# Performance work log

Hardware: AMD Instinct MI355X
Metric: run time of the kernel (lower is better)

## Reference

```python
import jax, jax.numpy as jnp
import numpy as np

# Model hyperparams (match init_kwargs)
D_MODEL = 1024
D_STATE = 128
D_CONV = 4
EXPAND = 2
HEADDIM = 64
NGROUPS = 1
D_INNER = EXPAND * D_MODEL          # 2048
D_SSM = D_INNER                     # d_ssm=None -> d_inner; d_mlp = 0
NHEADS = D_SSM // HEADDIM           # 32
CONV_DIM = D_SSM + 2 * NGROUPS * D_STATE            # 2304
D_IN_PROJ = 2 * D_INNER + 2 * NGROUPS * D_STATE + NHEADS  # 4384
GROUP_SIZE = D_SSM // NGROUPS
EPS = 1e-5
HEAD_TO_GROUP = np.arange(NHEADS) // (NHEADS // NGROUPS)


def silu(x):
    return x * jax.nn.sigmoid(x)


def setup_inputs() -> dict:
    key = jax.random.key(0)
    ks = jax.random.split(key, 10)
    B, L = 16, 512
    u = jax.random.normal(ks[0], (B, L, D_MODEL), jnp.float32)
    # in_proj (bias=False): weight [d_in_proj, d_model]
    W_in = jax.random.normal(ks[1], (D_IN_PROJ, D_MODEL), jnp.float32) / np.sqrt(D_MODEL)
    # depthwise causal conv1d: weight [conv_dim, 1, d_conv], bias [conv_dim]
    conv_w = jax.random.normal(ks[2], (CONV_DIM, 1, D_CONV), jnp.float32) / np.sqrt(D_CONV)
    conv_b = jax.random.normal(ks[3], (CONV_DIM,), jnp.float32) * 0.01
    # recurrent feedback weights (zero-init in torch; small random here to exercise the path)
    W_rxbc = jax.random.normal(ks[4], (CONV_DIM, D_SSM), jnp.float32) * (0.01 / np.sqrt(D_SSM))
    W_rdt = jax.random.normal(ks[5], (NHEADS, D_SSM), jnp.float32) * (0.01 / np.sqrt(D_SSM))
    # dt_bias = inverse-softplus of dt ~ U_log[1e-3, 1e-1]
    dt = jnp.exp(jax.random.uniform(ks[6], (NHEADS,)) * (np.log(0.1) - np.log(0.001)) + np.log(0.001))
    dt_bias = dt + jnp.log(-jnp.expm1(-dt))
    A_log = jnp.log(jax.random.uniform(ks[7], (NHEADS,), minval=1.0, maxval=16.0))
    D_param = jnp.ones((NHEADS,), jnp.float32)
    norm_w = jnp.ones((D_SSM,), jnp.float32)
    W_out = jax.random.normal(ks[8], (D_MODEL, D_INNER), jnp.float32) / np.sqrt(D_INNER)
    return dict(u=u, W_in=W_in, conv_w=conv_w, conv_b=conv_b, W_rxbc=W_rxbc,
                W_rdt=W_rdt, dt_bias=dt_bias, A_log=A_log, D_param=D_param,
                norm_w=norm_w, W_out=W_out)


def _forward(u, W_in, conv_w, conv_b, W_rxbc, W_rdt, dt_bias, A_log, D_param, norm_w, W_out):
    B, L, _ = u.shape
    zxbcdt = jnp.einsum('bld,ed->ble', u, W_in)  # [B,L,d_in_proj]; d_mlp=0 so no z0/x0
    z, xBC_u, dt_raw = jnp.split(zxbcdt, [D_SSM, D_SSM + CONV_DIM], axis=-1)
    # causal depthwise conv over time (torch Conv1d pad=d_conv-1, truncated to L)
    xp = jnp.pad(xBC_u, ((0, 0), (D_CONV - 1, 0), (0, 0)))
    xBC_conv = conv_b + sum(xp[:, k:k + L, :] * conv_w[:, 0, k] for k in range(D_CONV))
    A = -jnp.exp(A_log.astype(jnp.float32))  # [H]

    def step(carry, inp):
        state, y_prev = carry            # state: [B,H,P,N] f32, y_prev: [B,d_ssm]
        xBC_t, dt_t, z_t = inp
        xBC = silu(xBC_t + y_prev @ W_rxbc.T)        # recurrent xBC feedback
        dtr = silu(dt_t + y_prev @ W_rdt.T)          # recurrent dt feedback
        x_t = xBC[:, :D_SSM]
        Bv = xBC[:, D_SSM:D_SSM + NGROUPS * D_STATE]
        Cv = xBC[:, D_SSM + NGROUPS * D_STATE:]
        dt = jax.nn.softplus(dtr + dt_bias).astype(jnp.float32)  # [B,H]; dt_limit=(0,inf) -> no clamp
        dA = jnp.exp(dt * A)                                     # [B,H]
        x_h = x_t.reshape(B, NHEADS, HEADDIM).astype(jnp.float32)
        B_hn = Bv.reshape(B, NGROUPS, D_STATE).astype(jnp.float32)[:, HEAD_TO_GROUP, :]
        C_hn = Cv.reshape(B, NGROUPS, D_STATE).astype(jnp.float32)[:, HEAD_TO_GROUP, :]
        state = state * dA[:, :, None, None] + dt[:, :, None, None] * x_h[:, :, :, None] * B_hn[:, :, None, :]
        y = (state * C_hn[:, :, None, :]).sum(-1) + D_param[None, :, None] * x_h  # [B,H,P]
        y = y.reshape(B, D_SSM)
        # gated RMSNorm (norm_before_gate=False): rmsnorm(y*silu(z)) * weight, groupwise
        g = y * silu(z_t)
        gg = g.reshape(B, NGROUPS, GROUP_SIZE)
        ms = jnp.mean(gg * gg, axis=-1, keepdims=True)
        yn = (gg * jax.lax.rsqrt(ms + EPS)).reshape(B, D_SSM) * norm_w
        out_t = yn @ W_out.T
        return (state, yn), out_t

    state0 = jnp.zeros((B, NHEADS, HEADDIM, D_STATE), jnp.float32)
    y0 = jnp.zeros((B, D_SSM), u.dtype)
    xs = (jnp.swapaxes(xBC_conv, 0, 1), jnp.swapaxes(dt_raw, 0, 1), jnp.swapaxes(z, 0, 1))
    _, out = jax.lax.scan(step, (state0, y0), xs)  # out: [L,B,d_model]
    return jnp.swapaxes(out, 0, 1)


def reference(u, W_in, conv_w, conv_b, W_rxbc, W_rdt, dt_bias, A_log, D_param, norm_w, W_out):
    return _forward(u, W_in, conv_w, conv_b, W_rxbc, W_rdt, dt_bias, A_log, D_param, norm_w, W_out)
```

## Files before the change

### kernel.cpp

```cpp
#include <hip/hip_runtime.h>

typedef __attribute__((ext_vector_type(8))) short short8;
typedef __attribute__((ext_vector_type(4))) float floatx4;

#define BQ 16
#define LQ 512
#define DM 1024
#define DPROJ 4384
#define RAWC 2336
#define KD 2048
#define NWG 128
#define NTHR 512
#define AWG 73

#define RAWT_SLOT 37376
#define MSUM_SLOT 512

__device__ __forceinline__ float siluf(float x) { return x / (1.f + __expf(-x)); }
__device__ __forceinline__ float softplusf(float x) { return (x > 20.f) ? x : log1pf(__expf(x)); }
__device__ __forceinline__ unsigned short f2bf(float f) {
    union { float f; unsigned u; } v; v.f = f;
    unsigned r = v.u + 0x7FFFu + ((v.u >> 16) & 1u);
    return (unsigned short)(r >> 16);
}
__device__ __forceinline__ unsigned long long ld64(const unsigned long long* p) {
    return __hip_atomic_load(p, __ATOMIC_RELAXED, __HIP_MEMORY_SCOPE_AGENT);
}
__device__ __forceinline__ void st64(unsigned long long* p, unsigned long long v) {
    __hip_atomic_store(p, v, __ATOMIC_RELAXED, __HIP_MEMORY_SCOPE_AGENT);
}
__device__ __forceinline__ unsigned long long packf(float f, unsigned e) {
    union { float f; unsigned u; } v; v.f = f;
    return ((unsigned long long)e << 32) | v.u;
}
__device__ __forceinline__ float lof(unsigned long long w) {
    union { unsigned u; float f; } v; v.u = (unsigned)w; return v.f;
}
__device__ __forceinline__ unsigned hie(unsigned long long w) { return (unsigned)(w >> 32); }

__global__ void cvt_bf16_kernel(const float* __restrict__ s, unsigned short* __restrict__ d, int n) {
    int i = blockIdx.x * 256 + threadIdx.x;
    if (i < n) d[i] = f2bf(s[i]);
}

__global__ void pack_weights_kernel(const float* __restrict__ rxbc, const float* __restrict__ rdt,
                                    const float* __restrict__ wout, unsigned short* __restrict__ wall) {
    long i = (long)blockIdx.x * 256 + threadIdx.x;
    if (i >= 3360L * KD) return;
    int c = (int)(i >> 11), k = (int)(i & 2047);
    const float* src = (c < 2304) ? rxbc + (long)c * KD + k
                     : (c < 2336) ? rdt + (long)(c - 2304) * KD + k
                     :              wout + (long)(c - 2336) * KD + k;
    wall[i] = f2bf(*src);
}

__global__ void setup_zero_kernel(unsigned* __restrict__ z, long nz, unsigned* __restrict__ gh0) {
    long i = (long)blockIdx.x * 256 + threadIdx.x;
    const long stride = (long)gridDim.x * 256;
    for (long k = i; k < nz; k += stride) z[k] = 0u;
    if (i < 16384) gh0[i] = 0u;
}

__global__ __launch_bounds__(256) void gemm_inproj_kernel(const short* __restrict__ A,
                                                          const short* __restrict__ Bw,
                                                          float* __restrict__ C) {
    const int lane = threadIdx.x & 63, wave = threadIdx.x >> 6;
    const int row = lane & 15, q = lane >> 4;
    const long m0 = (long)blockIdx.x * 128 + wave * 16;
    const long n0 = (long)blockIdx.y * 32;
    const short* ap0 = A + (m0 + row) * DM + q * 8;
    const short* ap1 = ap0 + 64 * DM;
    const short* bp0 = Bw + (n0 + row) * DM + q * 8;
    const short* bp1 = bp0 + 16 * DM;
    floatx4 acc00 = {0.f,0.f,0.f,0.f}, acc01 = {0.f,0.f,0.f,0.f};
    floatx4 acc10 = {0.f,0.f,0.f,0.f}, acc11 = {0.f,0.f,0.f,0.f};
    for (int k = 0; k < DM; k += 32) {
        short8 a0 = *(const short8*)(ap0 + k);
        short8 a1 = *(const short8*)(ap1 + k);
        short8 b0 = *(const short8*)(bp0 + k);
        short8 b1 = *(const short8*)(bp1 + k);
        acc00 = __builtin_amdgcn_mfma_f32_16x16x32_bf16(a0, b0, acc00, 0, 0, 0);
        acc01 = __builtin_amdgcn_mfma_f32_16x16x32_bf16(a0, b1, acc01, 0, 0, 0);
        acc10 = __builtin_amdgcn_mfma_f32_16x16x32_bf16(a1, b0, acc10, 0, 0, 0);
        acc11 = __builtin_amdgcn_mfma_f32_16x16x32_bf16(a1, b1, acc11, 0, 0, 0);
    }
    float* cp0 = C + (m0 + q * 4) * DPROJ + n0 + row;
    float* cp1 = cp0 + 64 * DPROJ;
    #pragma unroll
    for (int r = 0; r < 4; ++r) {
        cp0[(long)r * DPROJ]      = acc00[r];
        cp0[(long)r * DPROJ + 16] = acc01[r];
        cp1[(long)r * DPROJ]      = acc10[r];
        cp1[(long)r * DPROJ + 16] = acc11[r];
    }
}

__global__ __launch_bounds__(NTHR, 1) void scan_kernel(
    const float* __restrict__ zx,
    unsigned long long* __restrict__ rawT,
    unsigned short* __restrict__ ghist,
    unsigned long long* __restrict__ msum,
    unsigned* __restrict__ bar,
    const short* __restrict__ wall,
    float* __restrict__ scale_hist,
    const float* __restrict__ dt_bias, const float* __restrict__ A_log,
    const float* __restrict__ D_param, const float* __restrict__ norm_w,
    const float* __restrict__ conv_w, const float* __restrict__ conv_b,
    float* __restrict__ out)
{
    const int w = blockIdx.x, tid = threadIdx.x;
    const int lane = tid & 63, wv = tid >> 6;

    __shared__ float redu[2][8][16][16];
    __shared__ float bc_lds[2][128];
    __shared__ float ypart[4][64];

    const bool doA = (w < AWG);
    const int colr = lane & 15, q = lane >> 4;
    const unsigned long long* gq = (const unsigned long long*)ghist;
    const int abase = colr * 512 + wv * 64 + q * 2;
    const int r_tl = tid >> 8, r_idx = tid & 255, r_orow = r_idx >> 4, r_col = r_idx & 15;
    const unsigned* aspin = bar + ((((lane >> 2) * 8 + wv) * 4) + (lane & 3)) * 32;

    short8 wr0[8], wr1[8];
    if (doA) {
        const short* wp0 = wall + ((long)((2 * w    ) * 16 + colr) * KD + wv * 256 + q * 8);
        const short* wp1 = wall + ((long)((2 * w + 1) * 16 + colr) * KD + wv * 256 + q * 8);
        #pragma unroll
        for (int ks = 0; ks < 8; ++ks) {
            wr0[ks] = *(const short8*)(wp0 + ks * 32);
            wr1[ks] = *(const short8*)(wp1 + ks * 32);
        }
    }

    const int b = w >> 3;
    const int j = w & 7;
    const int h = j * 4 + (wv >> 1);
    const int half = wv & 1;
    float s[64];
    #pragma unroll
    for (int i = 0; i < 64; ++i) s[i] = 0.f;
    const float Aneg = -__expf(A_log[h]);
    const float dtb  = dt_bias[h];
    const float Dp   = D_param[h];
    const float nw   = norm_w[h * 64 + lane];
    const int cx = h * 64 + lane;
    const float4 cwx = *(const float4*)(conv_w + cx * 4);
    const float cbx = conv_b[cx];
    const int bcw = tid >> 7, bcn = tid & 127;
    const int cbc = 2048 + bcw * 128 + bcn;
    float4 cwbc = {0.f,0.f,0.f,0.f}; float cbbc = 0.f;
    if (tid < 256) { cwbc = *(const float4*)(conv_w + cbc * 4); cbbc = conv_b[cbc]; }
    float xh1 = 0.f, xh2 = 0.f, xh3 = 0.f, bh1 = 0.f, bh2 = 0.f, bh3 = 0.f;

    for (int t = 0; t < LQ; ++t) {
        const unsigned eR = (unsigned)(t + 1);
        const long zr = ((long)b * LQ + t) * DPROJ;
        float xq  = zx[zr + 2048 + cx];
        float zq  = zx[zr + cx];
        float dzq = zx[zr + 4352 + h];
        float bq = 0.f;
        if (tid < 256) bq = zx[zr + 2048 + cbc];

        if (doA) {
            while (__hip_atomic_load(aspin, __ATOMIC_RELAXED, __HIP_MEMORY_SCOPE_AGENT)
                   < (unsigned)t) {}
            unsigned long long ar[16];
            const long gb0 = (long)t * 8192 + abase;
            #pragma unroll
            for (int ks = 0; ks < 8; ++ks) {
                ar[2 * ks]     = ld64(gq + gb0 + ks * 8);
                ar[2 * ks + 1] = ld64(gq + gb0 + ks * 8 + 1);
            }
            floatx4 acc0 = {0.f,0.f,0.f,0.f}, acc1 = {0.f,0.f,0.f,0.f};
            #pragma unroll
            for (int ks = 0; ks < 8; ++ks) {
                union { unsigned long long u[2]; short8 s8; } af;
                af.u[0] = ar[2 * ks]; af.u[1] = ar[2 * ks + 1];
                acc0 = __builtin_amdgcn_mfma_f32_16x16x32_bf16(af.s8, wr0[ks], acc0, 0, 0, 0);
                acc1 = __builtin_amdgcn_mfma_f32_16x16x32_bf16(af.s8, wr1[ks], acc1, 0, 0, 0);
            }
            #pragma unroll
            for (int r = 0; r < 4; ++r) {
                redu[0][wv][q * 4 + r][colr] = acc0[r];
                redu[1][wv][q * 4 + r][colr] = acc1[r];
            }
            __syncthreads();
            float v = 0.f;
            #pragma unroll
            for (int kq = 0; kq < 8; ++kq) v += redu[r_tl][kq][r_orow][r_col];
            const int gc = (2 * w + r_tl) * 16 + r_col;
            st64(rawT + (long)(t & 1) * RAWT_SLOT + r_orow * 2336 + gc, packf(v, eR));
        }

        const unsigned long long* rbase = rawT + (long)(t & 1) * RAWT_SLOT + (long)b * 2336;
        unsigned long long xw = ld64(rbase + cx);
        unsigned long long dw = ld64(rbase + 2304 + h);
        unsigned long long bw = 0;
        if (tid < 256) bw = ld64(rbase + cbc);
        float mv = 0.f;
        if (lane < 32) {
            const unsigned long long* mp = msum + ((t + 7) & 7) * MSUM_SLOT + b * 32 + lane;
            unsigned long long wd = ld64(mp);
            while (hie(wd) != (unsigned)t) wd = ld64(mp);
            mv = lof(wd);
        }
        float msv = mv;
        #pragma unroll
        for (int off = 32; off; off >>= 1) msv += __shfl_xor(msv, off, 64);
        const float rs = rsqrtf(msv * (1.f / 2048.f) + 1e-5f);
        if (j == 0 && tid == 0 && t >= 1)
            __hip_atomic_store(scale_hist + b * LQ + (t - 1), rs,
                               __ATOMIC_RELAXED, __HIP_MEMORY_SCOPE_AGENT);
        while (hie(xw) != eR) xw = ld64(rbase + cx);
        const float xr = lof(xw);
        while (hie(dw) != eR) dw = ld64(rbase + 2304 + h);
        const float dtrr = lof(dw);
        if (tid < 256) {
            while (hie(bw) != eR) bw = ld64(rbase + cbc);
            float bcval = lof(bw);
            float pre = cbbc + bh3 * cwbc.x + bh2 * cwbc.y + bh1 * cwbc.z + bq * cwbc.w;
            bc_lds[bcw][bcn] = siluf(pre + rs * bcval);
            bh3 = bh2; bh2 = bh1; bh1 = bq;
        }
        float xpre = cbx + xh3 * cwx.x + xh2 * cwx.y + xh1 * cwx.z + xq * cwx.w;
        xh3 = xh2; xh2 = xh1; xh1 = xq;
        float xv = siluf(xpre + rs * xr);
        float dt = softplusf(siluf(dzq + rs * dtrr) + dtb);
        float dA = __expf(dt * Aneg);
        float zg = siluf(zq);
        __syncthreads();

        float dtx = dt * xv, yac = 0.f;
        const floatx4* Bp = (const floatx4*)&bc_lds[0][half * 64];
        const floatx4* Cp = (const floatx4*)&bc_lds[1][half * 64];
        #pragma unroll
        for (int i = 0; i < 16; ++i) {
            floatx4 b4 = Bp[i], c4 = Cp[i];
            s[4*i+0] = s[4*i+0] * dA + dtx * b4.x; yac += s[4*i+0] * c4.x;
            s[4*i+1] = s[4*i+1] * dA + dtx * b4.y; yac += s[4*i+1] * c4.y;
            s[4*i+2] = s[4*i+2] * dA + dtx * b4.z; yac += s[4*i+2] * c4.z;
            s[4*i+3] = s[4*i+3] * dA + dtx * b4.w; yac += s[4*i+3] * c4.w;
        }
        if (half) ypart[wv >> 1][lane] = yac;
        __syncthreads();
        if (!half) {
            float y = yac + ypart[wv >> 1][lane] + Dp * xv;
            float g = y * zg;
            unsigned gb = (unsigned)f2bf(g * nw);
            unsigned up = __shfl_down(gb, 1);
            if (!(lane & 1))
                __hip_atomic_store((unsigned*)ghist + ((long)(t + 1) * 16384
                                   + ((b * KD + h * 64 + lane) >> 1)),
                                   gb | (up << 16), __ATOMIC_RELAXED, __HIP_MEMORY_SCOPE_AGENT);
            float sq = g * g;
            #pragma unroll
            for (int off = 32; off; off >>= 1) sq += __shfl_xor(sq, off, 64);
            if (lane == 0)
                st64(msum + ((t & 7) * MSUM_SLOT + b * 32 + j * 4 + (wv >> 1)), packf(sq, eR));
            asm volatile("s_waitcnt vmcnt(0)" ::: "memory");
            if (lane == 0)
                __hip_atomic_store(bar + (w * 4 + (wv >> 1)) * 32, (unsigned)(t + 1),
                                   __ATOMIC_RELAXED, __HIP_MEMORY_SCOPE_AGENT);
        }
    }

    {
        const unsigned* fp = bar + tid * 32;
        while (__hip_atomic_load(fp, __ATOMIC_RELAXED, __HIP_MEMORY_SCOPE_AGENT) < 512u) {}
    }
    __syncthreads();
    {
        const int vb = w * 2 + (tid >> 8);
        const int vt = tid & 255;
        const int vwv = vt >> 6, vlane = vt & 63;
        const int vcolr = vlane & 15, vq = vlane >> 4;
        const unsigned long long* gq2 = (const unsigned long long*)ghist;
        for (int it = 0; it < 8; ++it) {
            const int idx = vb * 8 + it;
            const int tt = idx >> 2;
            const int n0 = (idx & 3) * 256 + vwv * 64;
            const long ab = (long)(tt + 1) * 8192 + vcolr * 512 + vq * 2;
            const short* bp = wall + ((long)(2336 + n0 + vcolr) * KD + vq * 8);
            floatx4 acc0 = {0.f,0.f,0.f,0.f}, acc1 = {0.f,0.f,0.f,0.f};
            floatx4 acc2 = {0.f,0.f,0.f,0.f}, acc3 = {0.f,0.f,0.f,0.f};
            #pragma unroll 4
            for (int kb = 0; kb < 64; ++kb) {
                unsigned long long a0 = ld64(gq2 + ab + kb * 8);
                unsigned long long a1 = ld64(gq2 + ab + kb * 8 + 1);
                union { unsigned long long u[2]; short8 s8; } af;
                af.u[0] = a0; af.u[1] = a1;
                const short* bk = bp + kb * 32;
                acc0 = __builtin_amdgcn_mfma_f32_16x16x32_bf16(af.s8, *(const short8*)(bk),           acc0, 0, 0, 0);
                acc1 = __builtin_amdgcn_mfma_f32_16x16x32_bf16(af.s8, *(const short8*)(bk + 16 * KD), acc1, 0, 0, 0);
                acc2 = __builtin_amdgcn_mfma_f32_16x16x32_bf16(af.s8, *(const short8*)(bk + 32 * KD), acc2, 0, 0, 0);
                acc3 = __builtin_amdgcn_mfma_f32_16x16x32_bf16(af.s8, *(const short8*)(bk + 48 * KD), acc3, 0, 0, 0);
            }
            #pragma unroll
            for (int r = 0; r < 4; ++r) {
                const int bb = vq * 4 + r;
                float sc;
                if (tt < LQ - 1) {
                    sc = __hip_atomic_load(scale_hist + bb * LQ + tt,
                                           __ATOMIC_RELAXED, __HIP_MEMORY_SCOPE_AGENT);
                } else {
                    float msv = 0.f;
                    #pragma unroll
                    for (int k = 0; k < 32; ++k)
                        msv += lof(ld64(msum + 7 * MSUM_SLOT + bb * 32 + k));
                    sc = rsqrtf(msv * (1.f / 2048.f) + 1e-5f);
                }
                float* op = out + ((long)bb * LQ + tt) * DM + n0 + vcolr;
                op[0]  = acc0[r] * sc;
                op[16] = acc1[r] * sc;
                op[32] = acc2[r] * sc;
                op[48] = acc3[r] * sc;
            }
        }
    }
}

extern "C" void kernel_launch(void* const* d_in, const int* in_sizes, int n_in,
                              void* d_out, int out_size, void* d_ws, size_t ws_size,
                              hipStream_t stream) {
    const float* u       = (const float*)d_in[0];
    const float* W_in    = (const float*)d_in[1];
    const float* conv_w  = (const float*)d_in[2];
    const float* conv_b  = (const float*)d_in[3];
    const float* W_rxbc  = (const float*)d_in[4];
    const float* W_rdt   = (const float*)d_in[5];
    const float* dt_bias = (const float*)d_in[6];
    const float* A_log   = (const float*)d_in[7];
    const float* D_param = (const float*)d_in[8];
    const float* norm_w  = (const float*)d_in[9];
    const float* W_out   = (const float*)d_in[10];
    float* out = (float*)d_out;

    char* ws = (char*)d_ws;
    size_t off = 0;
    auto alloc = [&](size_t bytes) -> void* {
        void* p = ws + off; off += (bytes + 255) & ~(size_t)255; return p;
    };
    float* zx            = (float*)alloc((size_t)BQ * LQ * DPROJ * 4);
    unsigned short* u_bf = (unsigned short*)alloc((size_t)BQ * LQ * DM * 2);
    unsigned short* w_bf = (unsigned short*)alloc((size_t)DPROJ * DM * 2);
    unsigned short* gh   = (unsigned short*)alloc((size_t)(LQ + 1) * BQ * KD * 2);
    unsigned long long* rawT = (unsigned long long*)alloc((size_t)2 * RAWT_SLOT * 8);
    unsigned long long* msum = (unsigned long long*)alloc((size_t)8 * MSUM_SLOT * 8);
    unsigned* bar        = (unsigned*)alloc(16384 * 4);
    float* scale_hist    = (float*)alloc((size_t)BQ * LQ * 4);

    const long zero_u32 = ((size_t)2 * RAWT_SLOT * 8 + (size_t)8 * MSUM_SLOT * 8
                           + (size_t)16384 * 4) / 4;
    setup_zero_kernel<<<680, 256, 0, stream>>>((unsigned*)rawT, zero_u32, (unsigned*)gh);

    { int n = BQ * LQ * DM; cvt_bf16_kernel<<<(n + 255) / 256, 256, 0, stream>>>(u, u_bf, n); }
    { int n = DPROJ * DM;   cvt_bf16_kernel<<<(n + 255) / 256, 256, 0, stream>>>(W_in, w_bf, n); }
    gemm_inproj_kernel<<<dim3(BQ * LQ / 128, DPROJ / 32), 256, 0, stream>>>(
        (const short*)u_bf, (const short*)w_bf, zx);
    unsigned short* wall = u_bf;
    { long n = 3360L * KD;
      pack_weights_kernel<<<(int)((n + 255) / 256), 256, 0, stream>>>(W_rxbc, W_rdt, W_out, wall); }

    void* args[] = { &zx, &rawT, &gh, &msum, &bar, &wall, &scale_hist,
                     &dt_bias, &A_log, &D_param, &norm_w, &conv_w, &conv_b, &out };
    hipLaunchCooperativeKernel((void*)scan_kernel, dim3(NWG), dim3(NTHR), args, 0, stream);
}
```

Before: 5.754 ms.

## Split scan workgroup into dedicated recurrence and matvec wavefronts

Splits the 8 wavefronts per workgroup into two roles. Four wavefronts now each own one full head state (128 registers per lane), which removes the half-split ypart reduction. The other four wavefronts run the recurrent-feedback MFMA matvec over K=2048 and stream the weights from global memory each step instead of keeping them in registers. The next timestep's zx inputs are also prefetched after the step's barrier store. This trades higher per-lane register pressure and repeated weight loads for more specialised wavefronts and fewer LDS round trips on the serial critical path.

```diff
diff --git a/kernel.cpp b/kernel.cpp
--- a/kernel.cpp
+++ b/kernel.cpp
@@ -7,7 +7,6 @@
 #define LQ 512
 #define DM 1024
 #define DPROJ 4384
-#define RAWC 2336
 #define KD 2048
 #define NWG 128
 #define NTHR 512
@@ -111,35 +110,30 @@
     const int w = blockIdx.x, tid = threadIdx.x;
     const int lane = tid & 63, wv = tid >> 6;
 
-    __shared__ float redu[2][8][16][16];
+    __shared__ float redu[2][4][16][16];
     __shared__ float bc_lds[2][128];
-    __shared__ float ypart[4][64];
-
-    const bool doA = (w < AWG);
+
+    const bool isB = (wv < 4);
+    const bool isA = (wv >= 4) && (w < AWG);
     const int colr = lane & 15, q = lane >> 4;
     const unsigned long long* gq = (const unsigned long long*)ghist;
-    const int abase = colr * 512 + wv * 64 + q * 2;
-    const int r_tl = tid >> 8, r_idx = tid & 255, r_orow = r_idx >> 4, r_col = r_idx & 15;
-    const unsigned* aspin = bar + ((((lane >> 2) * 8 + wv) * 4) + (lane & 3)) * 32;
-
-    short8 wr0[8], wr1[8];
-    if (doA) {
-        const short* wp0 = wall + ((long)((2 * w    ) * 16 + colr) * KD + wv * 256 + q * 8);
-        const short* wp1 = wall + ((long)((2 * w + 1) * 16 + colr) * KD + wv * 256 + q * 8);
-        #pragma unroll
-        for (int ks = 0; ks < 8; ++ks) {
-            wr0[ks] = *(const short8*)(wp0 + ks * 32);
-            wr1[ks] = *(const short8*)(wp1 + ks * 32);
-        }
-    }
-
-    const int b = w >> 3;
-    const int j = w & 7;
-    const int h = j * 4 + (wv >> 1);
-    const int half = wv & 1;
-    float s[64];
+
+    const int m = isA ? (wv - 4) : 0;
+    const long gqb = (long)colr * 512 + m * 128 + q * 2;
+    const short* wp0 = wall + ((long)(w * 32 + colr) * KD + m * 512 + q * 8);
+    const short* wp1 = wp0 + 16 * KD;
+    const unsigned *af0, *af1;
+    {
+        const int c0 = 2 * lane, c1 = 2 * lane + 1;
+        af0 = bar + (((c0 >> 3) * 8 + 2 * m + ((c0 >> 2) & 1)) * 4 + (c0 & 3)) * 32;
+        af1 = bar + (((c1 >> 3) * 8 + 2 * m + ((c1 >> 2) & 1)) * 4 + (c1 & 3)) * 32;
+    }
+
+    const int b = w >> 3, j = w & 7;
+    const int h = j * 4 + (wv & 3);
+    float s[128];
     #pragma unroll
-    for (int i = 0; i < 64; ++i) s[i] = 0.f;
+    for (int i = 0; i < 128; ++i) s[i] = 0.f;
     const float Aneg = -__expf(A_log[h]);
     const float dtb  = dt_bias[h];
     const float Dp   = D_param[h];
@@ -147,105 +141,105 @@
     const int cx = h * 64 + lane;
     const float4 cwx = *(const float4*)(conv_w + cx * 4);
     const float cbx = conv_b[cx];
-    const int bcw = tid >> 7, bcn = tid & 127;
-    const int cbc = 2048 + bcw * 128 + bcn;
+    const int cbc = 2048 + (tid >> 7) * 128 + (tid & 127);
     float4 cwbc = {0.f,0.f,0.f,0.f}; float cbbc = 0.f;
-    if (tid < 256) { cwbc = *(const float4*)(conv_w + cbc * 4); cbbc = conv_b[cbc]; }
+    if (isB) { cwbc = *(const float4*)(conv_w + cbc * 4); cbbc = conv_b[cbc]; }
     float xh1 = 0.f, xh2 = 0.f, xh3 = 0.f, bh1 = 0.f, bh2 = 0.f, bh3 = 0.f;
+    float xq_c = 0.f, zq_c = 0.f, dzq_c = 0.f, bq_c = 0.f;
+    if (isB) {
+        const long zr0 = ((long)b * LQ) * DPROJ;
+        xq_c  = zx[zr0 + 2048 + cx];
+        zq_c  = zx[zr0 + cx];
+        dzq_c = zx[zr0 + 4352 + h];
+        bq_c  = zx[zr0 + 2048 + cbc];
+    }
 
     for (int t = 0; t < LQ; ++t) {
         const unsigned eR = (unsigned)(t + 1);
-        const long zr = ((long)b * LQ + t) * DPROJ;
-        float xq  = zx[zr + 2048 + cx];
-        float zq  = zx[zr + cx];
-        float dzq = zx[zr + 4352 + h];
-        float bq = 0.f;
-        if (tid < 256) bq = zx[zr + 2048 + cbc];
-
-        if (doA) {
-            while (__hip_atomic_load(aspin, __ATOMIC_RELAXED, __HIP_MEMORY_SCOPE_AGENT)
+
+        if (isA) {
+            while (__hip_atomic_load(af0, __ATOMIC_RELAXED, __HIP_MEMORY_SCOPE_AGENT)
                    < (unsigned)t) {}
-            unsigned long long ar[16];
-            const long gb0 = (long)t * 8192 + abase;
-            #pragma unroll
-            for (int ks = 0; ks < 8; ++ks) {
-                ar[2 * ks]     = ld64(gq + gb0 + ks * 8);
-                ar[2 * ks + 1] = ld64(gq + gb0 + ks * 8 + 1);
-            }
+            while (__hip_atomic_load(af1, __ATOMIC_RELAXED, __HIP_MEMORY_SCOPE_AGENT)
+                   < (unsigned)t) {}
+            const long gb0 = (long)t * 8192 + gqb;
             floatx4 acc0 = {0.f,0.f,0.f,0.f}, acc1 = {0.f,0.f,0.f,0.f};
             #pragma unroll
-            for (int ks = 0; ks < 8; ++ks) {
+            for (int ks = 0; ks < 16; ++ks) {
+                unsigned long long a0 = ld64(gq + gb0 + ks * 8);
+                unsigned long long a1 = ld64(gq + gb0 + ks * 8 + 1);
                 union { unsigned long long u[2]; short8 s8; } af;
-                af.u[0] = ar[2 * ks]; af.u[1] = ar[2 * ks + 1];
-                acc0 = __builtin_amdgcn_mfma_f32_16x16x32_bf16(af.s8, wr0[ks], acc0, 0, 0, 0);
-                acc1 = __builtin_amdgcn_mfma_f32_16x16x32_bf16(af.s8, wr1[ks], acc1, 0, 0, 0);
+                af.u[0] = a0; af.u[1] = a1;
+                short8 b0 = *(const short8*)(wp0 + ks * 32);
+                short8 b1 = *(const short8*)(wp1 + ks * 32);
+                acc0 = __builtin_amdgcn_mfma_f32_16x16x32_bf16(af.s8, b0, acc0, 0, 0, 0);
+                acc1 = __builtin_amdgcn_mfma_f32_16x16x32_bf16(af.s8, b1, acc1, 0, 0, 0);
             }
             #pragma unroll
             for (int r = 0; r < 4; ++r) {
-                redu[0][wv][q * 4 + r][colr] = acc0[r];
-                redu[1][wv][q * 4 + r][colr] = acc1[r];
-            }
-            __syncthreads();
+                redu[0][m][q * 4 + r][colr] = acc0[r];
+                redu[1][m][q * 4 + r][colr] = acc1[r];
+            }
+        }
+        __syncthreads();
+
+        float xv = 0.f, dt = 0.f, dA = 0.f, zg = 0.f;
+        if (w < AWG) {
+            const int orow = tid >> 5, ocol = tid & 31;
             float v = 0.f;
             #pragma unroll
-            for (int kq = 0; kq < 8; ++kq) v += redu[r_tl][kq][r_orow][r_col];
-            const int gc = (2 * w + r_tl) * 16 + r_col;
-            st64(rawT + (long)(t & 1) * RAWT_SLOT + r_orow * 2336 + gc, packf(v, eR));
-        }
-
-        const unsigned long long* rbase = rawT + (long)(t & 1) * RAWT_SLOT + (long)b * 2336;
-        unsigned long long xw = ld64(rbase + cx);
-        unsigned long long dw = ld64(rbase + 2304 + h);
-        unsigned long long bw = 0;
-        if (tid < 256) bw = ld64(rbase + cbc);
-        float mv = 0.f;
-        if (lane < 32) {
-            const unsigned long long* mp = msum + ((t + 7) & 7) * MSUM_SLOT + b * 32 + lane;
-            unsigned long long wd = ld64(mp);
-            while (hie(wd) != (unsigned)t) wd = ld64(mp);
-            mv = lof(wd);
-        }
-        float msv = mv;
-        #pragma unroll
-        for (int off = 32; off; off >>= 1) msv += __shfl_xor(msv, off, 64);
-        const float rs = rsqrtf(msv * (1.f / 2048.f) + 1e-5f);
-        if (j == 0 && tid == 0 && t >= 1)
-            __hip_atomic_store(scale_hist + b * LQ + (t - 1), rs,
-                               __ATOMIC_RELAXED, __HIP_MEMORY_SCOPE_AGENT);
-        while (hie(xw) != eR) xw = ld64(rbase + cx);
-        const float xr = lof(xw);
-        while (hie(dw) != eR) dw = ld64(rbase + 2304 + h);
-        const float dtrr = lof(dw);
-        if (tid < 256) {
+            for (int kw = 0; kw < 4; ++kw) v += redu[ocol >> 4][kw][orow][ocol & 15];
+            st64(rawT + (long)(t & 1) * RAWT_SLOT + orow * 2336 + w * 32 + ocol,
+                 packf(v, eR));
+        }
+        if (isB) {
+            const unsigned long long* rbase = rawT + (long)(t & 1) * RAWT_SLOT + (long)b * 2336;
+            unsigned long long xw = ld64(rbase + cx);
+            unsigned long long dw = ld64(rbase + 2304 + h);
+            unsigned long long bw = ld64(rbase + cbc);
+            float mv = 0.f;
+            if (lane < 32) {
+                const unsigned long long* mp = msum + ((t + 7) & 7) * MSUM_SLOT + b * 32 + lane;
+                unsigned long long wd = ld64(mp);
+                while (hie(wd) != (unsigned)t) wd = ld64(mp);
+                mv = lof(wd);
+            }
+            float msv = mv;
+            #pragma unroll
+            for (int off = 32; off; off >>= 1) msv += __shfl_xor(msv, off, 64);
+            const float rs = rsqrtf(msv * (1.f / 2048.f) + 1e-5f);
+            if (j == 0 && tid == 0 && t >= 1)
+                __hip_atomic_store(scale_hist + b * LQ + (t - 1), rs,
+                                   __ATOMIC_RELAXED, __HIP_MEMORY_SCOPE_AGENT);
+            while (hie(xw) != eR) xw = ld64(rbase + cx);
+            while (hie(dw) != eR) dw = ld64(rbase + 2304 + h);
             while (hie(bw) != eR) bw = ld64(rbase + cbc);
-            float bcval = lof(bw);
-            float pre = cbbc + bh3 * cwbc.x + bh2 * cwbc.y + bh1 * cwbc.z + bq * cwbc.w;
-            bc_lds[bcw][bcn] = siluf(pre + rs * bcval);
-            bh3 = bh2; bh2 = bh1; bh1 = bq;
-        }
-        float xpre = cbx + xh3 * cwx.x + xh2 * cwx.y + xh1 * cwx.z + xq * cwx.w;
-        xh3 = xh2; xh2 = xh1; xh1 = xq;
-        float xv = siluf(xpre + rs * xr);
-        float dt = softplusf(siluf(dzq + rs * dtrr) + dtb);
-        float dA = __expf(dt * Aneg);
-        float zg = siluf(zq);
+            const float xr = lof(xw), dtrr = lof(dw), bcval = lof(bw);
+            float pre = cbbc + bh3 * cwbc.x + bh2 * cwbc.y + bh1 * cwbc.z + bq_c * cwbc.w;
+            bc_lds[tid >> 7][tid & 127] = siluf(pre + rs * bcval);
+            bh3 = bh2; bh2 = bh1; bh1 = bq_c;
+            float xpre = cbx + xh3 * cwx.x + xh2 * cwx.y + xh1 * cwx.z + xq_c * cwx.w;
+            xh3 = xh2; xh2 = xh1; xh1 = xq_c;
+            xv = siluf(xpre + rs * xr);
+            dt = softplusf(siluf(dzq_c + rs * dtrr) + dtb);
+            dA = __expf(dt * Aneg);
+            zg = siluf(zq_c);
+        }
         __syncthreads();
 
-        float dtx = dt * xv, yac = 0.f;
-        const floatx4* Bp = (const floatx4*)&bc_lds[0][half * 64];
-        const floatx4* Cp = (const floatx4*)&bc_lds[1][half * 64];
-        #pragma unroll
-        for (int i = 0; i < 16; ++i) {
-            floatx4 b4 = Bp[i], c4 = Cp[i];
-            s[4*i+0] = s[4*i+0] * dA + dtx * b4.x; yac += s[4*i+0] * c4.x;
-            s[4*i+1] = s[4*i+1] * dA + dtx * b4.y; yac += s[4*i+1] * c4.y;
-            s[4*i+2] = s[4*i+2] * dA + dtx * b4.z; yac += s[4*i+2] * c4.z;
-            s[4*i+3] = s[4*i+3] * dA + dtx * b4.w; yac += s[4*i+3] * c4.w;
-        }
-        if (half) ypart[wv >> 1][lane] = yac;
-        __syncthreads();
-        if (!half) {
-            float y = yac + ypart[wv >> 1][lane] + Dp * xv;
+        if (isB) {
+            float dtx = dt * xv, yac = 0.f;
+            const floatx4* Bp = (const floatx4*)&bc_lds[0][0];
+            const floatx4* Cp = (const floatx4*)&bc_lds[1][0];
+            #pragma unroll
+            for (int i = 0; i < 32; ++i) {
+                floatx4 b4 = Bp[i], c4 = Cp[i];
+                s[4*i+0] = s[4*i+0] * dA + dtx * b4.x; yac += s[4*i+0] * c4.x;
+                s[4*i+1] = s[4*i+1] * dA + dtx * b4.y; yac += s[4*i+1] * c4.y;
+                s[4*i+2] = s[4*i+2] * dA + dtx * b4.z; yac += s[4*i+2] * c4.z;
+                s[4*i+3] = s[4*i+3] * dA + dtx * b4.w; yac += s[4*i+3] * c4.w;
+            }
+            float y = yac + Dp * xv;
             float g = y * zg;
             unsigned gb = (unsigned)f2bf(g * nw);
             unsigned up = __shfl_down(gb, 1);
@@ -257,11 +251,18 @@
             #pragma unroll
             for (int off = 32; off; off >>= 1) sq += __shfl_xor(sq, off, 64);
             if (lane == 0)
-                st64(msum + ((t & 7) * MSUM_SLOT + b * 32 + j * 4 + (wv >> 1)), packf(sq, eR));
+                st64(msum + ((t & 7) * MSUM_SLOT + b * 32 + j * 4 + wv), packf(sq, eR));
             asm volatile("s_waitcnt vmcnt(0)" ::: "memory");
             if (lane == 0)
-                __hip_atomic_store(bar + (w * 4 + (wv >> 1)) * 32, (unsigned)(t + 1),
+                __hip_atomic_store(bar + (w * 4 + wv) * 32, eR,
                                    __ATOMIC_RELAXED, __HIP_MEMORY_SCOPE_AGENT);
+            if (t + 1 < LQ) {
+                const long zr = ((long)b * LQ + (t + 1)) * DPROJ;
+                xq_c  = zx[zr + 2048 + cx];
+                zq_c  = zx[zr + cx];
+                dzq_c = zx[zr + 4352 + h];
+                bq_c  = zx[zr + 2048 + cbc];
+            }
         }
     }
 
```

Result: slower. 7.841 ms (+36.3%).
